# Performance work log

Measured on AMD Instinct MI355X. Metric: run time of the kernel, lower is better.

Reference implementation:

```python
import jax, jax.numpy as jnp
import numpy as np
from jax import lax

T, B, D, H = 512, 64, 256, 512  # time, batch, input_dim, hidden_dim


def setup_inputs() -> dict:
    key = jax.random.key(0)
    ks = jax.random.split(key, 9)
    fan_in = D + H
    s = 1.0 / np.sqrt(fan_in)
    inputs = jax.random.normal(ks[0], (T, B, D), dtype=jnp.float32)
    # torch nn.Linear weight layout: [out_features, in_features]
    Wf = jax.random.uniform(ks[1], (H, fan_in), jnp.float32, -s, s)
    bf = jax.random.uniform(ks[2], (H,), jnp.float32, -s, s)
    Wi = jax.random.uniform(ks[3], (H, fan_in), jnp.float32, -s, s)
    bi = jax.random.uniform(ks[4], (H,), jnp.float32, -s, s)
    Wg = jax.random.uniform(ks[5], (H, fan_in), jnp.float32, -s, s)
    bg = jax.random.uniform(ks[6], (H,), jnp.float32, -s, s)
    Wo = jax.random.uniform(ks[7], (H, fan_in), jnp.float32, -s, s)
    bo = jax.random.uniform(ks[8], (H,), jnp.float32, -s, s)
    return {"inputs": inputs, "Wf": Wf, "bf": bf, "Wi": Wi, "bi": bi,
            "Wg": Wg, "bg": bg, "Wo": Wo, "bo": bo}


def reference(inputs, Wf, bf, Wi, bi, Wg, bg, Wo, bo):
    # LSTM-style gated recurrence, n_qubits=0 path (no depth loop, proj_back = Identity)
    batch = inputs.shape[1]
    hidden = bf.shape[0]
    h0 = jnp.zeros((batch, hidden), inputs.dtype)
    c0 = jnp.zeros((batch, hidden), inputs.dtype)

    def step(carry, x):
        hx, cx = carry
        comb = jnp.concatenate([x, hx], axis=1)  # [B, D+H]
        f = jax.nn.sigmoid(comb @ Wf.T + bf)
        i = jax.nn.sigmoid(comb @ Wi.T + bi)
        g = jnp.tanh(comb @ Wg.T + bg)
        o = jax.nn.sigmoid(comb @ Wo.T + bo)
        cx = f * cx + i * g
        hx = o * jnp.tanh(cx)
        return (hx, cx), hx

    (hx, cx), outputs = lax.scan(step, (h0, c0), inputs)
    return outputs, hx, cx
```

## Files before the change

kernel.cpp:

```cpp
#include <hip/hip_runtime.h>
#include <stdint.h>

#define T_STEPS 512
#define BATCH   64
#define DIN     256
#define HID     512
#define KTOT    768
#define NTEAMS  4
#define TB      16
#define KK_X    8
#define KK_H    16
#define KK_ALL  24

#define POLL_BOUND (1 << 18)

typedef __bf16 v8bf __attribute__((ext_vector_type(8)));
typedef float  v4f  __attribute__((ext_vector_type(4)));
typedef unsigned int v4u __attribute__((ext_vector_type(4)));
typedef unsigned int v2u __attribute__((ext_vector_type(2)));

#define FLAGS_OFF 0
#define HBUF_OFF  8192
#define WPK_OFF   (HBUF_OFF + 131072)
#define XPK_OFF   (WPK_OFF + 3145728)

#define LOADX4_DEV(d, a, IMM) \
  asm volatile("global_load_dwordx4 %0, %1, off offset:" IMM " sc1" \
               : "=v"(d) : "v"(a) : "memory")
#define ST2_DEV(a, v) \
  asm volatile("global_store_dwordx2 %0, %1, off sc1" :: "v"(a), "v"(v) : "memory")
#define ST_DW_DEV(a, v) \
  asm volatile("global_store_dword %0, %1, off sc1" :: "v"(a), "v"(v) : "memory")
#define LOADX4(d, a) \
  asm volatile("global_load_dwordx4 %0, %1, off" : "=v"(d) : "v"(a) : "memory")
#define DRAIN_VM() asm volatile("s_waitcnt vmcnt(0)" ::: "memory")

static __device__ __forceinline__ unsigned int ld_flag_dev(const unsigned int* p) {
  unsigned int v;
  asm volatile("global_load_dword %0, %1, off sc1\n\ts_waitcnt vmcnt(0)"
               : "=v"(v) : "v"(p) : "memory");
  return v;
}

static __device__ __forceinline__ unsigned short f2bf(float x) {
  union { float f; uint32_t u; } v; v.f = x;
  uint32_t r = (v.u + 0x7fffu + ((v.u >> 16) & 1u)) >> 16;
  return (unsigned short)r;
}

static __device__ __forceinline__ float sigm(float x) {
  float e = __builtin_amdgcn_exp2f(-1.44269504f * x);
  return __builtin_amdgcn_rcpf(1.0f + e);
}
static __device__ __forceinline__ float tanh_(float x) {
  float e = __builtin_amdgcn_exp2f(2.88539008f * x);
  return 1.0f - 2.0f * __builtin_amdgcn_rcpf(e + 1.0f);
}

__global__ void pack_w(const float* __restrict__ Wf, const float* __restrict__ Wi,
                       const float* __restrict__ Wg, const float* __restrict__ Wo,
                       unsigned short* __restrict__ wpk) {
  int n = blockIdx.x * 256 + threadIdx.x;
  int l  = n & 63;
  int kk = (n >> 6) % KK_ALL;
  int wv = (n >> 6) / KK_ALL;
  int row  = l & 15;
  int gate = row & 3;
  int unit = (wv >> 2) * 16 + (wv & 3) * 4 + (row >> 2);
  int col  = kk * 32 + (l >> 4) * 8;
  const float* W = (gate == 0) ? Wf : (gate == 1) ? Wi : (gate == 2) ? Wg : Wo;
  const float* src = W + (size_t)unit * KTOT + col;
  unsigned short* dst = wpk + (size_t)n * 8;
#pragma unroll
  for (int e = 0; e < 8; e++) dst[e] = f2bf(src[e]);
}

__global__ void pack_x(const float* __restrict__ X, unsigned short* __restrict__ xpk) {
  int n = blockIdx.x * 256 + threadIdx.x;
  int l    = n & 63;
  int kk   = (n >> 6) & 7;
  int team = (n >> 9) & 3;
  int t    = n >> 11;
  int b    = team * TB + (l & 15);
  int col  = kk * 32 + (l >> 4) * 8;
  const float* src = X + ((size_t)(t * BATCH + b)) * DIN + col;
  unsigned short* dst = xpk + (size_t)n * 8;
#pragma unroll
  for (int e = 0; e < 8; e++) dst[e] = f2bf(src[e]);
}

__global__ void __launch_bounds__(256, 1)
lstm_rec(const float* __restrict__ bf_, const float* __restrict__ bi_,
         const float* __restrict__ bg_, const float* __restrict__ bo_,
         const unsigned short* __restrict__ wpk, const unsigned short* __restrict__ xpk,
         float* __restrict__ out, unsigned int* flags, unsigned short* hbuf) {
  int blk  = blockIdx.x;
  int team = blk & 7;
  if (team >= NTEAMS) return;
  int cu  = blk >> 3;
  int tid = threadIdx.x;
  int w   = tid >> 6, l = tid & 63;
  int brow = l & 15;
  int ul   = l >> 4;
  int u    = cu * 16 + w * 4 + ul;
  int bglob = team * TB + brow;

  __shared__ v4u hls[1024];
  char* hl = (char*)hls;

  v4u wfu[KK_ALL];
  {
    const char* wp = (const char*)(wpk + ((size_t)(cu * 4 + w)) * (KK_ALL * 512) + l * 8);
#pragma unroll
    for (int kk = 0; kk < KK_ALL; kk++) LOADX4(wfu[kk], wp + (size_t)kk * 1024);
    DRAIN_VM();
  }
  float b0 = bf_[u], b1 = bi_[u], b2 = bg_[u], b3 = bo_[u];
  float c = 0.0f, hval = 0.0f;

  char* slab0 = (char*)(hbuf + (size_t)team * 2 * (TB * HID));
  char* slab1 = slab0 + TB * HID * 2;

  unsigned int* ftm = flags + (size_t)team * 32 * 16;
  unsigned int* myflag = ftm + (size_t)cu * 16;

  float* outb = out + (size_t)bglob * HID + u;

  for (int t = 0; t < T_STEPS; t++) {
    v8bf xf[KK_X];
    {
      const v8bf* xp = (const v8bf*)(xpk + ((size_t)(t * NTEAMS + team)) * (KK_X * 512) + l * 8);
#pragma unroll
      for (int kk = 0; kk < KK_X; kk++) xf[kk] = xp[kk * 64];
    }

    if (t > 0) {
      if (w == 0) {
        const unsigned int* pp = ftm + (size_t)(l & 31) * 16;
        int guard = 0;
        while (true) {
          unsigned int v = ld_flag_dev(pp);
          if (__all(v >= (unsigned)t)) break;
          if (++guard > POLL_BOUND) break;
        }
      }
      __syncthreads();
    }

    v4u s0, s1, s2, s3;
    {
      const char* sb = ((t & 1) ? slab1 : slab0) + w * 4096 + l * 16;
      LOADX4_DEV(s0, sb, "0");
      LOADX4_DEV(s1, sb, "1024");
      LOADX4_DEV(s2, sb, "2048");
      LOADX4_DEV(s3, sb, "3072");
    }

    v4f acc[4];
    acc[0] = (v4f){b0, b1, b2, b3};
    acc[1] = (v4f){0.f, 0.f, 0.f, 0.f};
    acc[2] = (v4f){0.f, 0.f, 0.f, 0.f};
    acc[3] = (v4f){0.f, 0.f, 0.f, 0.f};
#pragma unroll
    for (int kk = 0; kk < KK_X; kk++)
      acc[kk & 3] = __builtin_amdgcn_mfma_f32_16x16x32_bf16(
          __builtin_bit_cast(v8bf, wfu[kk]), xf[kk], acc[kk & 3], 0, 0, 0);

    DRAIN_VM();
    __builtin_amdgcn_sched_barrier(0);

    {
      int r = w * 4;
      *(v4u*)(hl + (((r + 0) * 1024 + l * 16) ^ (((r + 0) & 7) << 4))) = s0;
      *(v4u*)(hl + (((r + 1) * 1024 + l * 16) ^ (((r + 1) & 7) << 4))) = s1;
      *(v4u*)(hl + (((r + 2) * 1024 + l * 16) ^ (((r + 2) & 7) << 4))) = s2;
      *(v4u*)(hl + (((r + 3) * 1024 + l * 16) ^ (((r + 3) & 7) << 4))) = s3;
    }
    __syncthreads();

#pragma unroll
    for (int kk = 0; kk < KK_H; kk++) {
      int off = (brow * 1024 + kk * 64 + ul * 16) ^ ((brow & 7) << 4);
      v8bf hf = *(const v8bf*)(hl + off);
      acc[kk & 3] = __builtin_amdgcn_mfma_f32_16x16x32_bf16(
          __builtin_bit_cast(v8bf, wfu[KK_X + kk]), hf, acc[kk & 3], 0, 0, 0);
    }
    v4f g4 = (acc[0] + acc[1]) + (acc[2] + acc[3]);

    float fg = sigm(g4[0]);
    float ig = sigm(g4[1]);
    float gg = tanh_(g4[2]);
    float og = sigm(g4[3]);
    c    = fg * c + ig * gg;
    hval = og * tanh_(c);

    if (t < T_STEPS - 1) {
      float h0 = __shfl(hval, brow);
      float h1 = __shfl(hval, brow + 16);
      float h2 = __shfl(hval, brow + 32);
      float h3 = __shfl(hval, brow + 48);
      if (l < 16) {
        v2u pk;
        pk.x = (unsigned)f2bf(h0) | ((unsigned)f2bf(h1) << 16);
        pk.y = (unsigned)f2bf(h2) | ((unsigned)f2bf(h3) << 16);
        char* pd = (((t + 1) & 1) ? slab1 : slab0) + brow * 1024 + cu * 32 + w * 8;
        ST2_DEV(pd, pk);
      }
      DRAIN_VM();
      __syncthreads();
      if (tid == 0) ST_DW_DEV(myflag, (unsigned)(t + 1));
    }

    outb[(size_t)t * (BATCH * HID)] = hval;
  }

  float* hx = out + (size_t)T_STEPS * BATCH * HID;
  hx[(size_t)bglob * HID + u] = hval;
  float* cx = hx + BATCH * HID;
  cx[(size_t)bglob * HID + u] = c;
}

extern "C" void kernel_launch(void* const* d_in, const int* in_sizes, int n_in,
                              void* d_out, int out_size, void* d_ws, size_t ws_size,
                              hipStream_t stream) {
  const float* X  = (const float*)d_in[0];
  const float* Wf = (const float*)d_in[1];
  const float* bf = (const float*)d_in[2];
  const float* Wi = (const float*)d_in[3];
  const float* bi = (const float*)d_in[4];
  const float* Wg = (const float*)d_in[5];
  const float* bg = (const float*)d_in[6];
  const float* Wo = (const float*)d_in[7];
  const float* bo = (const float*)d_in[8];
  float* out = (float*)d_out;
  char* ws = (char*)d_ws;

  unsigned int*   flags = (unsigned int*)(ws + FLAGS_OFF);
  unsigned short* hbuf  = (unsigned short*)(ws + HBUF_OFF);
  unsigned short* wpk   = (unsigned short*)(ws + WPK_OFF);
  unsigned short* xpk   = (unsigned short*)(ws + XPK_OFF);

  hipMemsetAsync(ws, 0, WPK_OFF, stream);
  pack_w<<<768, 256, 0, stream>>>(Wf, Wi, Wg, Wo, wpk);
  pack_x<<<4096, 256, 0, stream>>>(X, xpk);
  lstm_rec<<<256, 256, 0, stream>>>(bf, bi, bg, bo, wpk, xpk, out, flags, hbuf);
}
```

Baseline: 1.348 ms.

## Replace flag-based step sync with step-tagged hidden-state words polled directly

Result: slower. 1.998 ms (+48.2%).

```diff
diff --git a/kernel.cpp b/kernel.cpp
--- a/kernel.cpp
+++ b/kernel.cpp
@@ -17,30 +17,19 @@
 typedef __bf16 v8bf __attribute__((ext_vector_type(8)));
 typedef float  v4f  __attribute__((ext_vector_type(4)));
 typedef unsigned int v4u __attribute__((ext_vector_type(4)));
-typedef unsigned int v2u __attribute__((ext_vector_type(2)));
-
-#define FLAGS_OFF 0
-#define HBUF_OFF  8192
-#define WPK_OFF   (HBUF_OFF + 131072)
+
+#define HBUF_OFF  0
+#define WPK_OFF   262144
 #define XPK_OFF   (WPK_OFF + 3145728)
 
 #define LOADX4_DEV(d, a, IMM) \
   asm volatile("global_load_dwordx4 %0, %1, off offset:" IMM " sc1" \
                : "=v"(d) : "v"(a) : "memory")
-#define ST2_DEV(a, v) \
-  asm volatile("global_store_dwordx2 %0, %1, off sc1" :: "v"(a), "v"(v) : "memory")
-#define ST_DW_DEV(a, v) \
-  asm volatile("global_store_dword %0, %1, off sc1" :: "v"(a), "v"(v) : "memory")
+#define ST4_DEV(a, v) \
+  asm volatile("global_store_dwordx4 %0, %1, off sc1" :: "v"(a), "v"(v) : "memory")
 #define LOADX4(d, a) \
   asm volatile("global_load_dwordx4 %0, %1, off" : "=v"(d) : "v"(a) : "memory")
 #define DRAIN_VM() asm volatile("s_waitcnt vmcnt(0)" ::: "memory")
-
-static __device__ __forceinline__ unsigned int ld_flag_dev(const unsigned int* p) {
-  unsigned int v;
-  asm volatile("global_load_dword %0, %1, off sc1\n\ts_waitcnt vmcnt(0)"
-               : "=v"(v) : "v"(p) : "memory");
-  return v;
-}
 
 static __device__ __forceinline__ unsigned short f2bf(float x) {
   union { float f; uint32_t u; } v; v.f = x;
@@ -93,7 +82,7 @@
 lstm_rec(const float* __restrict__ bf_, const float* __restrict__ bi_,
          const float* __restrict__ bg_, const float* __restrict__ bo_,
          const unsigned short* __restrict__ wpk, const unsigned short* __restrict__ xpk,
-         float* __restrict__ out, unsigned int* flags, unsigned short* hbuf) {
+         float* __restrict__ out, unsigned int* hbuf) {
   int blk  = blockIdx.x;
   int team = blk & 7;
   if (team >= NTEAMS) return;
@@ -105,8 +94,7 @@
   int u    = cu * 16 + w * 4 + ul;
   int bglob = team * TB + brow;
 
-  __shared__ v4u hls[1024];
-  char* hl = (char*)hls;
+  __shared__ v4u hls[2048];
 
   v4u wfu[KK_ALL];
   {
@@ -118,11 +106,11 @@
   float b0 = bf_[u], b1 = bi_[u], b2 = bg_[u], b3 = bo_[u];
   float c = 0.0f, hval = 0.0f;
 
-  char* slab0 = (char*)(hbuf + (size_t)team * 2 * (TB * HID));
-  char* slab1 = slab0 + TB * HID * 2;
-
-  unsigned int* ftm = flags + (size_t)team * 32 * 16;
-  unsigned int* myflag = ftm + (size_t)cu * 16;
+  unsigned int* slab0 = hbuf + (size_t)team * 2 * (TB * HID);
+  unsigned int* slab1 = slab0 + TB * HID;
+
+  int srow = w * 4 + (l >> 4);
+  int scol = l & 15;
 
   float* outb = out + (size_t)bglob * HID + u;
 
@@ -132,28 +120,6 @@
       const v8bf* xp = (const v8bf*)(xpk + ((size_t)(t * NTEAMS + team)) * (KK_X * 512) + l * 8);
 #pragma unroll
       for (int kk = 0; kk < KK_X; kk++) xf[kk] = xp[kk * 64];
-    }
-
-    if (t > 0) {
-      if (w == 0) {
-        const unsigned int* pp = ftm + (size_t)(l & 31) * 16;
-        int guard = 0;
-        while (true) {
-          unsigned int v = ld_flag_dev(pp);
-          if (__all(v >= (unsigned)t)) break;
-          if (++guard > POLL_BOUND) break;
-        }
-      }
-      __syncthreads();
-    }
-
-    v4u s0, s1, s2, s3;
-    {
-      const char* sb = ((t & 1) ? slab1 : slab0) + w * 4096 + l * 16;
-      LOADX4_DEV(s0, sb, "0");
-      LOADX4_DEV(s1, sb, "1024");
-      LOADX4_DEV(s2, sb, "2048");
-      LOADX4_DEV(s3, sb, "3072");
     }
 
     v4f acc[4];
@@ -166,15 +132,65 @@
       acc[kk & 3] = __builtin_amdgcn_mfma_f32_16x16x32_bf16(
           __builtin_bit_cast(v8bf, wfu[kk]), xf[kk], acc[kk & 3], 0, 0, 0);
 
-    DRAIN_VM();
-    __builtin_amdgcn_sched_barrier(0);
-
+    const unsigned int* sb = ((t & 1) ? slab1 : slab0) + (size_t)srow * HID + scol * 32;
+    v4u p0, p1, p2, p3, p4, p5, p6, p7;
+    if (t > 0) {
+      unsigned int tg = (unsigned)t;
+      int guard = 0;
+      while (true) {
+        LOADX4_DEV(p0, sb, "0");   LOADX4_DEV(p1, sb, "16");
+        LOADX4_DEV(p2, sb, "32");  LOADX4_DEV(p3, sb, "48");
+        LOADX4_DEV(p4, sb, "64");  LOADX4_DEV(p5, sb, "80");
+        LOADX4_DEV(p6, sb, "96");  LOADX4_DEV(p7, sb, "112");
+        DRAIN_VM();
+        __builtin_amdgcn_sched_barrier(0);
+        unsigned int m;
+        m  = (p0.x ^ tg) | (p0.y ^ tg) | (p0.z ^ tg) | (p0.w ^ tg);
+        m |= (p1.x ^ tg) | (p1.y ^ tg) | (p1.z ^ tg) | (p1.w ^ tg);
+        m |= (p2.x ^ tg) | (p2.y ^ tg) | (p2.z ^ tg) | (p2.w ^ tg);
+        m |= (p3.x ^ tg) | (p3.y ^ tg) | (p3.z ^ tg) | (p3.w ^ tg);
+        m |= (p4.x ^ tg) | (p4.y ^ tg) | (p4.z ^ tg) | (p4.w ^ tg);
+        m |= (p5.x ^ tg) | (p5.y ^ tg) | (p5.z ^ tg) | (p5.w ^ tg);
+        m |= (p6.x ^ tg) | (p6.y ^ tg) | (p6.z ^ tg) | (p6.w ^ tg);
+        m |= (p7.x ^ tg) | (p7.y ^ tg) | (p7.z ^ tg) | (p7.w ^ tg);
+        m &= 0xFFFFu;
+        if (__all(m == 0)) break;
+        if (++guard > POLL_BOUND) break;
+      }
+    } else {
+      LOADX4_DEV(p0, sb, "0");   LOADX4_DEV(p1, sb, "16");
+      LOADX4_DEV(p2, sb, "32");  LOADX4_DEV(p3, sb, "48");
+      LOADX4_DEV(p4, sb, "64");  LOADX4_DEV(p5, sb, "80");
+      LOADX4_DEV(p6, sb, "96");  LOADX4_DEV(p7, sb, "112");
+      DRAIN_VM();
+      __builtin_amdgcn_sched_barrier(0);
+    }
+
+    char* hl = (char*)hls + (t & 1) * 16384;
     {
-      int r = w * 4;
-      *(v4u*)(hl + (((r + 0) * 1024 + l * 16) ^ (((r + 0) & 7) << 4))) = s0;
-      *(v4u*)(hl + (((r + 1) * 1024 + l * 16) ^ (((r + 1) & 7) << 4))) = s1;
-      *(v4u*)(hl + (((r + 2) * 1024 + l * 16) ^ (((r + 2) & 7) << 4))) = s2;
-      *(v4u*)(hl + (((r + 3) * 1024 + l * 16) ^ (((r + 3) & 7) << 4))) = s3;
+      const unsigned int SEL = 0x07060302u;
+      int ob = (srow * 1024 + scol * 64) ^ ((srow & 7) << 4);
+      v4u o;
+      o.x = __builtin_amdgcn_perm(p0.y, p0.x, SEL);
+      o.y = __builtin_amdgcn_perm(p0.w, p0.z, SEL);
+      o.z = __builtin_amdgcn_perm(p1.y, p1.x, SEL);
+      o.w = __builtin_amdgcn_perm(p1.w, p1.z, SEL);
+      *(v4u*)(hl + (ob ^ 0)) = o;
+      o.x = __builtin_amdgcn_perm(p2.y, p2.x, SEL);
+      o.y = __builtin_amdgcn_perm(p2.w, p2.z, SEL);
+      o.z = __builtin_amdgcn_perm(p3.y, p3.x, SEL);
+      o.w = __builtin_amdgcn_perm(p3.w, p3.z, SEL);
+      *(v4u*)(hl + (ob ^ 16)) = o;
+      o.x = __builtin_amdgcn_perm(p4.y, p4.x, SEL);
+      o.y = __builtin_amdgcn_perm(p4.w, p4.z, SEL);
+      o.z = __builtin_amdgcn_perm(p5.y, p5.x, SEL);
+      o.w = __builtin_amdgcn_perm(p5.w, p5.z, SEL);
+      *(v4u*)(hl + (ob ^ 32)) = o;
+      o.x = __builtin_amdgcn_perm(p6.y, p6.x, SEL);
+      o.y = __builtin_amdgcn_perm(p6.w, p6.z, SEL);
+      o.z = __builtin_amdgcn_perm(p7.y, p7.x, SEL);
+      o.w = __builtin_amdgcn_perm(p7.w, p7.z, SEL);
+      *(v4u*)(hl + (ob ^ 48)) = o;
     }
     __syncthreads();
 
@@ -195,20 +211,20 @@
     hval = og * tanh_(c);
 
     if (t < T_STEPS - 1) {
-      float h0 = __shfl(hval, brow);
-      float h1 = __shfl(hval, brow + 16);
-      float h2 = __shfl(hval, brow + 32);
-      float h3 = __shfl(hval, brow + 48);
+      float a0 = __shfl(hval, brow);
+      float a1 = __shfl(hval, brow + 16);
+      float a2 = __shfl(hval, brow + 32);
+      float a3 = __shfl(hval, brow + 48);
       if (l < 16) {
-        v2u pk;
-        pk.x = (unsigned)f2bf(h0) | ((unsigned)f2bf(h1) << 16);
-        pk.y = (unsigned)f2bf(h2) | ((unsigned)f2bf(h3) << 16);
-        char* pd = (((t + 1) & 1) ? slab1 : slab0) + brow * 1024 + cu * 32 + w * 8;
-        ST2_DEV(pd, pk);
+        unsigned int tg = (unsigned)(t + 1);
+        v4u pk;
+        pk.x = ((unsigned)f2bf(a0) << 16) | tg;
+        pk.y = ((unsigned)f2bf(a1) << 16) | tg;
+        pk.z = ((unsigned)f2bf(a2) << 16) | tg;
+        pk.w = ((unsigned)f2bf(a3) << 16) | tg;
+        unsigned int* pd = (((t + 1) & 1) ? slab1 : slab0) + (size_t)brow * HID + cu * 16 + w * 4;
+        ST4_DEV(pd, pk);
       }
-      DRAIN_VM();
-      __syncthreads();
-      if (tid == 0) ST_DW_DEV(myflag, (unsigned)(t + 1));
     }
 
     outb[(size_t)t * (BATCH * HID)] = hval;
@@ -235,13 +251,12 @@
   float* out = (float*)d_out;
   char* ws = (char*)d_ws;
 
-  unsigned int*   flags = (unsigned int*)(ws + FLAGS_OFF);
-  unsigned short* hbuf  = (unsigned short*)(ws + HBUF_OFF);
-  unsigned short* wpk   = (unsigned short*)(ws + WPK_OFF);
-  unsigned short* xpk   = (unsigned short*)(ws + XPK_OFF);
+  unsigned int*   hbuf = (unsigned int*)(ws + HBUF_OFF);
+  unsigned short* wpk  = (unsigned short*)(ws + WPK_OFF);
+  unsigned short* xpk  = (unsigned short*)(ws + XPK_OFF);
 
   hipMemsetAsync(ws, 0, WPK_OFF, stream);
   pack_w<<<768, 256, 0, stream>>>(Wf, Wi, Wg, Wo, wpk);
   pack_x<<<4096, 256, 0, stream>>>(X, xpk);
-  lstm_rec<<<256, 256, 0, stream>>>(bf, bi, bg, bo, wpk, xpk, out, flags, hbuf);
-}
+  lstm_rec<<<256, 256, 0, stream>>>(bf, bi, bg, bo, wpk, xpk, out, hbuf);
+}
```

## Use per-wave flags and double-buffered LDS to drop block barriers

Applied to the files above, without the earlier changes.

Measured after the change: 3.387 ms. 2.51x slower.

```diff
diff --git a/kernel.cpp b/kernel.cpp
--- a/kernel.cpp
+++ b/kernel.cpp
@@ -20,12 +20,15 @@
 typedef unsigned int v2u __attribute__((ext_vector_type(2)));
 
 #define FLAGS_OFF 0
-#define HBUF_OFF  8192
+#define HBUF_OFF  4096
 #define WPK_OFF   (HBUF_OFF + 131072)
 #define XPK_OFF   (WPK_OFF + 3145728)
 
 #define LOADX4_DEV(d, a, IMM) \
   asm volatile("global_load_dwordx4 %0, %1, off offset:" IMM " sc1" \
+               : "=v"(d) : "v"(a) : "memory")
+#define LOADX2_DEV_W(d, a) \
+  asm volatile("global_load_dwordx2 %0, %1, off sc1\n\ts_waitcnt vmcnt(0)" \
                : "=v"(d) : "v"(a) : "memory")
 #define ST2_DEV(a, v) \
   asm volatile("global_store_dwordx2 %0, %1, off sc1" :: "v"(a), "v"(v) : "memory")
@@ -34,13 +37,6 @@
 #define LOADX4(d, a) \
   asm volatile("global_load_dwordx4 %0, %1, off" : "=v"(d) : "v"(a) : "memory")
 #define DRAIN_VM() asm volatile("s_waitcnt vmcnt(0)" ::: "memory")
-
-static __device__ __forceinline__ unsigned int ld_flag_dev(const unsigned int* p) {
-  unsigned int v;
-  asm volatile("global_load_dword %0, %1, off sc1\n\ts_waitcnt vmcnt(0)"
-               : "=v"(v) : "v"(p) : "memory");
-  return v;
-}
 
 static __device__ __forceinline__ unsigned short f2bf(float x) {
   union { float f; uint32_t u; } v; v.f = x;
@@ -105,8 +101,7 @@
   int u    = cu * 16 + w * 4 + ul;
   int bglob = team * TB + brow;
 
-  __shared__ v4u hls[1024];
-  char* hl = (char*)hls;
+  __shared__ v4u hls[2048];
 
   v4u wfu[KK_ALL];
   {
@@ -121,8 +116,9 @@
   char* slab0 = (char*)(hbuf + (size_t)team * 2 * (TB * HID));
   char* slab1 = slab0 + TB * HID * 2;
 
-  unsigned int* ftm = flags + (size_t)team * 32 * 16;
-  unsigned int* myflag = ftm + (size_t)cu * 16;
+  unsigned int* ftm = flags + (size_t)team * 128;
+  unsigned int* myflag = ftm + (size_t)(cu * 4 + w);
+  const unsigned int* fp = ftm + 2 * l;
 
   float* outb = out + (size_t)bglob * HID + u;
 
@@ -135,16 +131,15 @@
     }
 
     if (t > 0) {
-      if (w == 0) {
-        const unsigned int* pp = ftm + (size_t)(l & 31) * 16;
-        int guard = 0;
-        while (true) {
-          unsigned int v = ld_flag_dev(pp);
-          if (__all(v >= (unsigned)t)) break;
-          if (++guard > POLL_BOUND) break;
-        }
+      unsigned int tg = (unsigned)t;
+      int guard = 0;
+      while (true) {
+        v2u fv;
+        LOADX2_DEV_W(fv, fp);
+        __builtin_amdgcn_sched_barrier(0);
+        if (__all(fv.x >= tg && fv.y >= tg)) break;
+        if (++guard > POLL_BOUND) break;
       }
-      __syncthreads();
     }
 
     v4u s0, s1, s2, s3;
@@ -169,6 +164,7 @@
     DRAIN_VM();
     __builtin_amdgcn_sched_barrier(0);
 
+    char* hl = (char*)hls + (t & 1) * 16384;
     {
       int r = w * 4;
       *(v4u*)(hl + (((r + 0) * 1024 + l * 16) ^ (((r + 0) & 7) << 4))) = s0;
@@ -207,8 +203,7 @@
         ST2_DEV(pd, pk);
       }
       DRAIN_VM();
-      __syncthreads();
-      if (tid == 0) ST_DW_DEV(myflag, (unsigned)(t + 1));
+      if (l == 0) ST_DW_DEV(myflag, (unsigned)(t + 1));
     }
 
     outb[(size_t)t * (BATCH * HID)] = hval;
```

## Use per-step hidden slabs and XCD detection to skip cache-coherent loads

Applied to the files above, without the earlier changes.

After: 1.631 ms. 1.21x slower.

```diff
diff --git a/kernel.cpp b/kernel.cpp
--- a/kernel.cpp
+++ b/kernel.cpp
@@ -13,6 +13,7 @@
 #define KK_ALL  24
 
 #define POLL_BOUND (1 << 18)
+#define DET_BOUND  (1 << 20)
 
 typedef __bf16 v8bf __attribute__((ext_vector_type(8)));
 typedef float  v4f  __attribute__((ext_vector_type(4)));
@@ -20,19 +21,36 @@
 typedef unsigned int v2u __attribute__((ext_vector_type(2)));
 
 #define FLAGS_OFF 0
-#define HBUF_OFF  8192
-#define WPK_OFF   (HBUF_OFF + 131072)
+#define XCDB_OFF  8192
+#define XCNT_OFF  8704
+#define WPK_OFF   16384
 #define XPK_OFF   (WPK_OFF + 3145728)
+#define HBUF_OFF  (XPK_OFF + 16777216)
+#define WS_NEED   ((size_t)HBUF_OFF + 33554432u)
+#define FLAGS5_OFF 0
+#define HBUF5_OFF  8192
+#define WPK5_OFF   (HBUF5_OFF + 131072)
+#define XPK5_OFF   (WPK5_OFF + 3145728)
 
 #define LOADX4_DEV(d, a, IMM) \
   asm volatile("global_load_dwordx4 %0, %1, off offset:" IMM " sc1" \
                : "=v"(d) : "v"(a) : "memory")
+#define LOADX4_PLAIN(d, a, IMM) \
+  asm volatile("global_load_dwordx4 %0, %1, off offset:" IMM \
+               : "=v"(d) : "v"(a) : "memory")
 #define ST2_DEV(a, v) \
   asm volatile("global_store_dwordx2 %0, %1, off sc1" :: "v"(a), "v"(v) : "memory")
+#define ST2_PLAIN(a, v) \
+  asm volatile("global_store_dwordx2 %0, %1, off" :: "v"(a), "v"(v) : "memory")
 #define ST_DW_DEV(a, v) \
   asm volatile("global_store_dword %0, %1, off sc1" :: "v"(a), "v"(v) : "memory")
+#define ST_DW_SYS(a, v) \
+  asm volatile("global_store_dword %0, %1, off sc0 sc1" :: "v"(a), "v"(v) : "memory")
 #define LOADX4(d, a) \
   asm volatile("global_load_dwordx4 %0, %1, off" : "=v"(d) : "v"(a) : "memory")
+#define LOAD_DW_NB(d, a) \
+  asm volatile("global_load_dword %0, %1, off sc1" : "=v"(d) : "v"(a) : "memory")
+#define WAIT1() asm volatile("s_waitcnt vmcnt(1)" ::: "memory")
 #define DRAIN_VM() asm volatile("s_waitcnt vmcnt(0)" ::: "memory")
 
 static __device__ __forceinline__ unsigned int ld_flag_dev(const unsigned int* p) {
@@ -41,13 +59,18 @@
                : "=v"(v) : "v"(p) : "memory");
   return v;
 }
+static __device__ __forceinline__ unsigned int ld_dword_sys(const unsigned int* p) {
+  unsigned int v;
+  asm volatile("global_load_dword %0, %1, off sc0 sc1\n\ts_waitcnt vmcnt(0)"
+               : "=v"(v) : "v"(p) : "memory");
+  return v;
+}
 
 static __device__ __forceinline__ unsigned short f2bf(float x) {
   union { float f; uint32_t u; } v; v.f = x;
   uint32_t r = (v.u + 0x7fffu + ((v.u >> 16) & 1u)) >> 16;
   return (unsigned short)r;
 }
-
 static __device__ __forceinline__ float sigm(float x) {
   float e = __builtin_amdgcn_exp2f(-1.44269504f * x);
   return __builtin_amdgcn_rcpf(1.0f + e);
@@ -90,10 +113,11 @@
 }
 
 __global__ void __launch_bounds__(256, 1)
-lstm_rec(const float* __restrict__ bf_, const float* __restrict__ bi_,
-         const float* __restrict__ bg_, const float* __restrict__ bo_,
-         const unsigned short* __restrict__ wpk, const unsigned short* __restrict__ xpk,
-         float* __restrict__ out, unsigned int* flags, unsigned short* hbuf) {
+lstm_mono(const float* __restrict__ bf_, const float* __restrict__ bi_,
+          const float* __restrict__ bg_, const float* __restrict__ bo_,
+          const unsigned short* __restrict__ wpk, const unsigned short* __restrict__ xpk,
+          float* __restrict__ out, unsigned int* flags, unsigned int* xcdb,
+          unsigned int* xcnt, unsigned short* hbuf) {
   int blk  = blockIdx.x;
   int team = blk & 7;
   if (team >= NTEAMS) return;
@@ -105,8 +129,31 @@
   int u    = cu * 16 + w * 4 + ul;
   int bglob = team * TB + brow;
 
-  __shared__ v4u hls[1024];
-  char* hl = (char*)hls;
+  __shared__ v4u hls[2048];
+  __shared__ int mode_sh;
+
+  {
+    unsigned int* xb = xcdb + team * 32;
+    unsigned int* xc = xcnt + team * 16;
+    if (w == 0) {
+      if (l == 0) {
+        unsigned int myx;
+        asm volatile("s_getreg_b32 %0, hwreg(HW_REG_XCC_ID)" : "=s"(myx));
+        ST_DW_SYS(xb + cu, myx + 1u);
+        DRAIN_VM();
+        __hip_atomic_fetch_add(xc, 1u, __ATOMIC_RELEASE, __HIP_MEMORY_SCOPE_AGENT);
+        int guard = 0;
+        while (__hip_atomic_load(xc, __ATOMIC_ACQUIRE, __HIP_MEMORY_SCOPE_AGENT) < 32u) {
+          if (++guard > DET_BOUND) break;
+        }
+      }
+      unsigned int xv = ld_dword_sys(xb + (l & 31));
+      int ok = (__all(xv == __shfl(xv, 0)) && __shfl(xv, 0) != 0u) ? 1 : 0;
+      if (l == 0) mode_sh = ok;
+    }
+    __syncthreads();
+  }
+  const int fastsc = mode_sh;
 
   v4u wfu[KK_ALL];
   {
@@ -117,9 +164,6 @@
   }
   float b0 = bf_[u], b1 = bi_[u], b2 = bg_[u], b3 = bo_[u];
   float c = 0.0f, hval = 0.0f;
-
-  char* slab0 = (char*)(hbuf + (size_t)team * 2 * (TB * HID));
-  char* slab1 = slab0 + TB * HID * 2;
 
   unsigned int* ftm = flags + (size_t)team * 32 * 16;
   unsigned int* myflag = ftm + (size_t)cu * 16;
@@ -134,6 +178,151 @@
       for (int kk = 0; kk < KK_X; kk++) xf[kk] = xp[kk * 64];
     }
 
+    v4f acc[4];
+    acc[0] = (v4f){b0, b1, b2, b3};
+    acc[1] = (v4f){0.f, 0.f, 0.f, 0.f};
+    acc[2] = (v4f){0.f, 0.f, 0.f, 0.f};
+    acc[3] = (v4f){0.f, 0.f, 0.f, 0.f};
+#pragma unroll
+    for (int kk = 0; kk < KK_X; kk++)
+      acc[kk & 3] = __builtin_amdgcn_mfma_f32_16x16x32_bf16(
+          __builtin_bit_cast(v8bf, wfu[kk]), xf[kk], acc[kk & 3], 0, 0, 0);
+
+    if (t > 0) {
+      if (w == 0) {
+        const unsigned int* pp = ftm + (size_t)(l & 31) * 16;
+        unsigned int tg = (unsigned)t;
+        unsigned int fa, fb;
+        LOAD_DW_NB(fa, pp);
+        int guard = 0;
+        while (true) {
+          LOAD_DW_NB(fb, pp);
+          WAIT1();
+          __builtin_amdgcn_sched_barrier(0);
+          if (__all(fa >= tg)) break;
+          LOAD_DW_NB(fa, pp);
+          WAIT1();
+          __builtin_amdgcn_sched_barrier(0);
+          if (__all(fb >= tg)) break;
+          if ((guard += 2) > POLL_BOUND) break;
+        }
+      }
+      __syncthreads();
+
+      const char* slab_t = (const char*)(hbuf + ((size_t)t * NTEAMS + team) * (TB * HID));
+      const char* sb = slab_t + w * 4096 + l * 16;
+      v4u s0, s1, s2, s3;
+      if (fastsc) {
+        LOADX4_PLAIN(s0, sb, "0");
+        LOADX4_PLAIN(s1, sb, "1024");
+        LOADX4_PLAIN(s2, sb, "2048");
+        LOADX4_PLAIN(s3, sb, "3072");
+      } else {
+        LOADX4_DEV(s0, sb, "0");
+        LOADX4_DEV(s1, sb, "1024");
+        LOADX4_DEV(s2, sb, "2048");
+        LOADX4_DEV(s3, sb, "3072");
+      }
+      DRAIN_VM();
+      __builtin_amdgcn_sched_barrier(0);
+
+      char* hl = (char*)hls + (t & 1) * 16384;
+      {
+        int r = w * 4;
+        *(v4u*)(hl + (((r + 0) * 1024 + l * 16) ^ (((r + 0) & 7) << 4))) = s0;
+        *(v4u*)(hl + (((r + 1) * 1024 + l * 16) ^ (((r + 1) & 7) << 4))) = s1;
+        *(v4u*)(hl + (((r + 2) * 1024 + l * 16) ^ (((r + 2) & 7) << 4))) = s2;
+        *(v4u*)(hl + (((r + 3) * 1024 + l * 16) ^ (((r + 3) & 7) << 4))) = s3;
+      }
+      __syncthreads();
+
+#pragma unroll
+      for (int kk = 0; kk < KK_H; kk++) {
+        int off = (brow * 1024 + kk * 64 + ul * 16) ^ ((brow & 7) << 4);
+        v8bf hf = *(const v8bf*)(hl + off);
+        acc[kk & 3] = __builtin_amdgcn_mfma_f32_16x16x32_bf16(
+            __builtin_bit_cast(v8bf, wfu[KK_X + kk]), hf, acc[kk & 3], 0, 0, 0);
+      }
+    }
+
+    v4f g4 = (acc[0] + acc[1]) + (acc[2] + acc[3]);
+    float fg = sigm(g4[0]);
+    float ig = sigm(g4[1]);
+    float gg = tanh_(g4[2]);
+    float og = sigm(g4[3]);
+    c    = fg * c + ig * gg;
+    hval = og * tanh_(c);
+
+    if (t < T_STEPS - 1) {
+      float h0 = __shfl(hval, brow);
+      float h1 = __shfl(hval, brow + 16);
+      float h2 = __shfl(hval, brow + 32);
+      float h3 = __shfl(hval, brow + 48);
+      char* slab_n = (char*)(hbuf + ((size_t)(t + 1) * NTEAMS + team) * (TB * HID));
+      if (l < 16) {
+        v2u pk;
+        pk.x = (unsigned)f2bf(h0) | ((unsigned)f2bf(h1) << 16);
+        pk.y = (unsigned)f2bf(h2) | ((unsigned)f2bf(h3) << 16);
+        char* pd = slab_n + brow * 1024 + cu * 32 + w * 8;
+        if (fastsc) { ST2_PLAIN(pd, pk); } else { ST2_DEV(pd, pk); }
+      }
+      outb[(size_t)t * (BATCH * HID)] = hval;
+      DRAIN_VM();
+      __syncthreads();
+      if (tid == 0) ST_DW_DEV(myflag, (unsigned)(t + 1));
+    } else {
+      outb[(size_t)t * (BATCH * HID)] = hval;
+    }
+  }
+
+  float* hx = out + (size_t)T_STEPS * BATCH * HID;
+  hx[(size_t)bglob * HID + u] = hval;
+  float* cx = hx + BATCH * HID;
+  cx[(size_t)bglob * HID + u] = c;
+}
+
+__global__ void __launch_bounds__(256, 1)
+lstm_rec_r5(const float* __restrict__ bf_, const float* __restrict__ bi_,
+            const float* __restrict__ bg_, const float* __restrict__ bo_,
+            const unsigned short* __restrict__ wpk, const unsigned short* __restrict__ xpk,
+            float* __restrict__ out, unsigned int* flags, unsigned short* hbuf) {
+  int blk  = blockIdx.x;
+  int team = blk & 7;
+  if (team >= NTEAMS) return;
+  int cu  = blk >> 3;
+  int tid = threadIdx.x;
+  int w   = tid >> 6, l = tid & 63;
+  int brow = l & 15;
+  int ul   = l >> 4;
+  int u    = cu * 16 + w * 4 + ul;
+  int bglob = team * TB + brow;
+
+  __shared__ v4u hls[1024];
+  char* hl = (char*)hls;
+
+  v4u wfu[KK_ALL];
+  {
+    const char* wp = (const char*)(wpk + ((size_t)(cu * 4 + w)) * (KK_ALL * 512) + l * 8);
+#pragma unroll
+    for (int kk = 0; kk < KK_ALL; kk++) LOADX4(wfu[kk], wp + (size_t)kk * 1024);
+    DRAIN_VM();
+  }
+  float b0 = bf_[u], b1 = bi_[u], b2 = bg_[u], b3 = bo_[u];
+  float c = 0.0f, hval = 0.0f;
+
+  char* slab0 = (char*)(hbuf + (size_t)team * 2 * (TB * HID));
+  char* slab1 = slab0 + TB * HID * 2;
+  unsigned int* ftm = flags + (size_t)team * 32 * 16;
+  unsigned int* myflag = ftm + (size_t)cu * 16;
+  float* outb = out + (size_t)bglob * HID + u;
+
+  for (int t = 0; t < T_STEPS; t++) {
+    v8bf xf[KK_X];
+    {
+      const v8bf* xp = (const v8bf*)(xpk + ((size_t)(t * NTEAMS + team)) * (KK_X * 512) + l * 8);
+#pragma unroll
+      for (int kk = 0; kk < KK_X; kk++) xf[kk] = xp[kk * 64];
+    }
     if (t > 0) {
       if (w == 0) {
         const unsigned int* pp = ftm + (size_t)(l & 31) * 16;
@@ -146,7 +335,6 @@
       }
       __syncthreads();
     }
-
     v4u s0, s1, s2, s3;
     {
       const char* sb = ((t & 1) ? slab1 : slab0) + w * 4096 + l * 16;
@@ -155,7 +343,6 @@
       LOADX4_DEV(s2, sb, "2048");
       LOADX4_DEV(s3, sb, "3072");
     }
-
     v4f acc[4];
     acc[0] = (v4f){b0, b1, b2, b3};
     acc[1] = (v4f){0.f, 0.f, 0.f, 0.f};
@@ -165,10 +352,8 @@
     for (int kk = 0; kk < KK_X; kk++)
       acc[kk & 3] = __builtin_amdgcn_mfma_f32_16x16x32_bf16(
           __builtin_bit_cast(v8bf, wfu[kk]), xf[kk], acc[kk & 3], 0, 0, 0);
-
     DRAIN_VM();
     __builtin_amdgcn_sched_barrier(0);
-
     {
       int r = w * 4;
       *(v4u*)(hl + (((r + 0) * 1024 + l * 16) ^ (((r + 0) & 7) << 4))) = s0;
@@ -177,7 +362,6 @@
       *(v4u*)(hl + (((r + 3) * 1024 + l * 16) ^ (((r + 3) & 7) << 4))) = s3;
     }
     __syncthreads();
-
 #pragma unroll
     for (int kk = 0; kk < KK_H; kk++) {
       int off = (brow * 1024 + kk * 64 + ul * 16) ^ ((brow & 7) << 4);
@@ -186,14 +370,12 @@
           __builtin_bit_cast(v8bf, wfu[KK_X + kk]), hf, acc[kk & 3], 0, 0, 0);
     }
     v4f g4 = (acc[0] + acc[1]) + (acc[2] + acc[3]);
-
     float fg = sigm(g4[0]);
     float ig = sigm(g4[1]);
     float gg = tanh_(g4[2]);
     float og = sigm(g4[3]);
     c    = fg * c + ig * gg;
     hval = og * tanh_(c);
-
     if (t < T_STEPS - 1) {
       float h0 = __shfl(hval, brow);
       float h1 = __shfl(hval, brow + 16);
@@ -210,10 +392,8 @@
       __syncthreads();
       if (tid == 0) ST_DW_DEV(myflag, (unsigned)(t + 1));
     }
-
     outb[(size_t)t * (BATCH * HID)] = hval;
   }
-
   float* hx = out + (size_t)T_STEPS * BATCH * HID;
   hx[(size_t)bglob * HID + u] = hval;
   float* cx = hx + BATCH * HID;
@@ -235,13 +415,26 @@
   float* out = (float*)d_out;
   char* ws = (char*)d_ws;
 
-  unsigned int*   flags = (unsigned int*)(ws + FLAGS_OFF);
-  unsigned short* hbuf  = (unsigned short*)(ws + HBUF_OFF);
-  unsigned short* wpk   = (unsigned short*)(ws + WPK_OFF);
-  unsigned short* xpk   = (unsigned short*)(ws + XPK_OFF);
-
-  hipMemsetAsync(ws, 0, WPK_OFF, stream);
-  pack_w<<<768, 256, 0, stream>>>(Wf, Wi, Wg, Wo, wpk);
-  pack_x<<<4096, 256, 0, stream>>>(X, xpk);
-  lstm_rec<<<256, 256, 0, stream>>>(bf, bi, bg, bo, wpk, xpk, out, flags, hbuf);
-}
+  if (ws_size >= WS_NEED) {
+    unsigned int*   flags = (unsigned int*)(ws + FLAGS_OFF);
+    unsigned int*   xcdb  = (unsigned int*)(ws + XCDB_OFF);
+    unsigned int*   xcnt  = (unsigned int*)(ws + XCNT_OFF);
+    unsigned short* wpk   = (unsigned short*)(ws + WPK_OFF);
+    unsigned short* xpk   = (unsigned short*)(ws + XPK_OFF);
+    unsigned short* hbuf  = (unsigned short*)(ws + HBUF_OFF);
+    hipMemsetAsync(ws, 0, WPK_OFF, stream);
+    pack_w<<<768, 256, 0, stream>>>(Wf, Wi, Wg, Wo, wpk);
+    pack_x<<<4096, 256, 0, stream>>>(X, xpk);
+    lstm_mono<<<256, 256, 0, stream>>>(bf, bi, bg, bo, wpk, xpk, out,
+                                       flags, xcdb, xcnt, hbuf);
+  } else {
+    unsigned int*   flags = (unsigned int*)(ws + FLAGS5_OFF);
+    unsigned short* hbuf  = (unsigned short*)(ws + HBUF5_OFF);
+    unsigned short* wpk   = (unsigned short*)(ws + WPK5_OFF);
+    unsigned short* xpk   = (unsigned short*)(ws + XPK5_OFF);
+    hipMemsetAsync(ws, 0, WPK5_OFF, stream);
+    pack_w<<<768, 256, 0, stream>>>(Wf, Wi, Wg, Wo, wpk);
+    pack_x<<<4096, 256, 0, stream>>>(X, xpk);
+    lstm_rec_r5<<<256, 256, 0, stream>>>(bf, bi, bg, bo, wpk, xpk, out, flags, hbuf);
+  }
+}
```
